# Kernel optimization log

Hardware: AMD Instinct MI355X
Metric: run time of the kernel (lower is better)

## Reference

```python
import jax, jax.numpy as jnp
import numpy as np

N, M, D = 8192, 8192, 512

def setup_inputs() -> dict:
    key = jax.random.key(0)
    kx, ky = jax.random.split(key)
    X = jax.random.normal(kx, (N, D), dtype=jnp.float32)
    Y = jax.random.normal(ky, (M, D), dtype=jnp.float32)
    gamma = jnp.float32(1.0)  # learnable scalar kernel width
    return {"X": X, "Y": Y, "gamma": gamma}

def reference(X, Y, gamma):
    # RBF kernel: exp(-gamma * ||x_i - y_j||^2)
    x2 = jnp.sum(X * X, axis=-1)            # [n]
    y2 = jnp.sum(Y * Y, axis=-1)            # [m]
    xy = jnp.einsum('nd,md->nm', X, Y)      # [n, m] GEMM
    sq = x2[:, None] + y2[None, :] - 2.0 * xy
    sq = jnp.maximum(sq, 0.0)               # clamp tiny negatives from fp error
    return jnp.exp(-gamma * sq)
```

## Files before the change

kernel.cpp:

```cpp
#include <hip/hip_runtime.h>
#include <hip/hip_bf16.h>


#define NROWS 8192
#define D_DIM 512
#define BM 256
#define BN 256
#define BK 64
#define NKT (D_DIM / BK)

using bf16x8 = __attribute__((ext_vector_type(8))) short;
using f32x4  = __attribute__((ext_vector_type(4))) float;

__device__ inline unsigned pack2_bf16(float a, float b) {
    unsigned ua = __builtin_bit_cast(unsigned, a);
    unsigned ub = __builtin_bit_cast(unsigned, b);
    ua = (ua + 0x7fffu + ((ua >> 16) & 1u)) >> 16;
    ub = (ub + 0x7fffu + ((ub >> 16) & 1u)) >> 16;
    return ua | (ub << 16);
}

__global__ __launch_bounds__(64) void prep_kernel(const float* __restrict__ src,
                                                  unsigned short* __restrict__ dst,
                                                  float* __restrict__ norms) {
    const int row  = blockIdx.x;
    const int lane = threadIdx.x;
    const float4* s = reinterpret_cast<const float4*>(src) + (size_t)row * (D_DIM / 4);
    float4 v0 = s[lane * 2];
    float4 v1 = s[lane * 2 + 1];
    float ss = v0.x * v0.x + v0.y * v0.y + v0.z * v0.z + v0.w * v0.w +
               v1.x * v1.x + v1.y * v1.y + v1.z * v1.z + v1.w * v1.w;
    uint4 p;
    p.x = pack2_bf16(v0.x, v0.y);
    p.y = pack2_bf16(v0.z, v0.w);
    p.z = pack2_bf16(v1.x, v1.y);
    p.w = pack2_bf16(v1.z, v1.w);
    reinterpret_cast<uint4*>(dst + (size_t)row * D_DIM)[lane] = p;
    #pragma unroll
    for (int off = 32; off; off >>= 1) ss += __shfl_down(ss, off);
    if (lane == 0) norms[row] = ss;
}

__device__ inline void gload_lds16(const unsigned short* g, unsigned short* l) {
    __builtin_amdgcn_global_load_lds(
        (const __attribute__((address_space(1))) void*)g,
        (__attribute__((address_space(3))) void*)l, 16, 0, 0);
}

#define VMCNT(n) asm volatile("s_waitcnt vmcnt(" #n ")" ::: "memory")
#define BAR()    asm volatile("s_barrier" ::: "memory")
#define LDF(p)   (*reinterpret_cast<const bf16x8*>(p))
#define MFMA(a, b, c) __builtin_amdgcn_mfma_f32_16x16x32_bf16(a, b, c, 0, 0, 0)

__global__ __launch_bounds__(512, 2) void rbf_gemm(
    const unsigned short* __restrict__ Xb, const unsigned short* __restrict__ Yb,
    const float* __restrict__ x2, const float* __restrict__ y2,
    const float* __restrict__ gptr, float* __restrict__ out) {
    __shared__ unsigned short sA[2][BM * BK];
    __shared__ unsigned short sB[2][BN * BK];

    const int bid  = blockIdx.x;
    const int swz  = (bid & 7) * 128 + (bid >> 3);
    const int brow = swz >> 5;
    const int bcol = swz & 31;

    const int tid  = threadIdx.x;
    const int lane = tid & 63;
    const int wid  = tid >> 6;
    const int wr   = wid >> 2;
    const int wc   = wid & 3;

    const int slot  = tid & 7;
    const int srowA = tid >> 3;
    const int srowB = ((tid >> 3) & 31) + ((tid >> 8) << 6);
    const int scol  = (slot ^ ((tid >> 3) & 7)) * 8;
    const unsigned short* gA = Xb + (size_t)(brow * BM + srowA) * D_DIM + scol;
    const unsigned short* gB = Yb + (size_t)(bcol * BN + srowB) * D_DIM + scol;
    const int loffA = srowA * BK + slot * 8;
    const int loffB = srowB * BK + slot * 8;

    auto stA = [&](int d, int kt, int odd) {
        const unsigned short* g = gA + (size_t)(odd * 64) * D_DIM + kt * BK;
        unsigned short* l = sA[d] + odd * 64 * BK + loffA;
        gload_lds16(g, l);
        gload_lds16(g + 128 * D_DIM, l + 128 * BK);
    };
    auto stB = [&](int d, int kt, int odd) {
        const unsigned short* g = gB + (size_t)(odd * 32) * D_DIM + kt * BK;
        unsigned short* l = sB[d] + odd * 32 * BK + loffB;
        gload_lds16(g, l);
        gload_lds16(g + 128 * D_DIM, l + 128 * BK);
    };

    const int lr  = lane & 15;
    const int kg  = lane >> 4;
    const int lx  = lane & 7;
    const int sl0 = ((0 * 4 + kg) ^ lx) * 8;
    const int sl1 = ((1 * 4 + kg) ^ lx) * 8;
    const int aBase = (wr * 128 + lr) * BK;
    const int bBase = (wc * 64 + lr) * BK;

    f32x4 acc[8][4] = {};
    bf16x8 av[4][2], bv[4][2];

    stA(0, 0, 0); stB(0, 0, 0); stB(0, 0, 1); stA(0, 0, 1);
    VMCNT(4);
    BAR();

    for (int t = 0; t < NKT; ++t) {
        const int c = t & 1, d = c ^ 1;
        const bool pre = (t + 1 < NKT);
        const unsigned short* A = sA[c];
        const unsigned short* B = sB[c];

        #pragma unroll
        for (int m = 0; m < 4; ++m) {
            av[m][0] = LDF(A + aBase + m * 16 * BK + sl0);
            av[m][1] = LDF(A + aBase + m * 16 * BK + sl1);
        }
        #pragma unroll
        for (int n = 0; n < 2; ++n) {
            bv[n][0] = LDF(B + bBase + n * 16 * BK + sl0);
            bv[n][1] = LDF(B + bBase + n * 16 * BK + sl1);
        }
        if (pre) { stA(d, t + 1, 0); VMCNT(4); }
        else     { VMCNT(2); }
        BAR();
        __builtin_amdgcn_s_setprio(1);
        #pragma unroll
        for (int m = 0; m < 4; ++m)
            #pragma unroll
            for (int n = 0; n < 2; ++n) {
                acc[m][n] = MFMA(av[m][0], bv[n][0], acc[m][n]);
                acc[m][n] = MFMA(av[m][1], bv[n][1], acc[m][n]);
            }
        __builtin_amdgcn_s_setprio(0);

        #pragma unroll
        for (int n = 2; n < 4; ++n) {
            bv[n][0] = LDF(B + bBase + n * 16 * BK + sl0);
            bv[n][1] = LDF(B + bBase + n * 16 * BK + sl1);
        }
        if (pre) { stB(d, t + 1, 0); VMCNT(4); }
        else     { VMCNT(0); }
        BAR();
        __builtin_amdgcn_s_setprio(1);
        #pragma unroll
        for (int m = 0; m < 4; ++m)
            #pragma unroll
            for (int n = 2; n < 4; ++n) {
                acc[m][n] = MFMA(av[m][0], bv[n][0], acc[m][n]);
                acc[m][n] = MFMA(av[m][1], bv[n][1], acc[m][n]);
            }
        __builtin_amdgcn_s_setprio(0);

        #pragma unroll
        for (int m = 0; m < 4; ++m) {
            av[m][0] = LDF(A + aBase + (m + 4) * 16 * BK + sl0);
            av[m][1] = LDF(A + aBase + (m + 4) * 16 * BK + sl1);
        }
        if (pre) stB(d, t + 1, 1);
        BAR();
        __builtin_amdgcn_s_setprio(1);
        #pragma unroll
        for (int m = 0; m < 4; ++m)
            #pragma unroll
            for (int n = 0; n < 2; ++n) {
                acc[m + 4][n] = MFMA(av[m][0], bv[n][0], acc[m + 4][n]);
                acc[m + 4][n] = MFMA(av[m][1], bv[n][1], acc[m + 4][n]);
            }
        __builtin_amdgcn_s_setprio(0);

        if (pre) {
            stA(d, t + 1, 1);
            VMCNT(4);
            BAR();
        }
        __builtin_amdgcn_s_setprio(1);
        #pragma unroll
        for (int m = 0; m < 4; ++m)
            #pragma unroll
            for (int n = 2; n < 4; ++n) {
                acc[m + 4][n] = MFMA(av[m][0], bv[n][0], acc[m + 4][n]);
                acc[m + 4][n] = MFMA(av[m][1], bv[n][1], acc[m + 4][n]);
            }
        __builtin_amdgcn_s_setprio(0);
    }

    const float g = *gptr;
    const int rbase = brow * BM + wr * 128 + (kg << 2);
    const int cbase = bcol * BN + wc * 64 + lr;

    float yv[4];
    #pragma unroll
    for (int n = 0; n < 4; ++n) yv[n] = y2[cbase + n * 16];

    #pragma unroll
    for (int m = 0; m < 8; ++m) {
        #pragma unroll
        for (int r = 0; r < 4; ++r) {
            const float xr = x2[rbase + m * 16 + r];
            const size_t ro = (size_t)(rbase + m * 16 + r) * NROWS + cbase;
            #pragma unroll
            for (int n = 0; n < 4; ++n) {
                float sq = fmaxf(xr + yv[n] - 2.0f * acc[m][n][r], 0.0f);
                __builtin_nontemporal_store(__expf(-g * sq), &out[ro + n * 16]);
            }
        }
    }
}

extern "C" void kernel_launch(void* const* d_in, const int* in_sizes, int n_in,
                              void* d_out, int out_size, void* d_ws, size_t ws_size,
                              hipStream_t stream) {
    const float* X = (const float*)d_in[0];
    const float* Y = (const float*)d_in[1];
    const float* gamma = (const float*)d_in[2];
    float* out = (float*)d_out;

    unsigned short* Xb = (unsigned short*)d_ws;
    unsigned short* Yb = Xb + (size_t)NROWS * D_DIM;
    float* x2 = (float*)(Yb + (size_t)NROWS * D_DIM);
    float* y2 = x2 + NROWS;

    prep_kernel<<<NROWS, 64, 0, stream>>>(X, Xb, x2);
    prep_kernel<<<NROWS, 64, 0, stream>>>(Y, Yb, y2);

    const int grid = (NROWS / BM) * (NROWS / BN);
    rbf_gemm<<<grid, 512, 0, stream>>>(Xb, Yb, x2, y2, gamma, out);
}
```

Baseline: 355.8 us.

## Deepen global-to-LDS prefetch pipeline and merge X/Y prep kernels

Reworks the GEMM main loop so LDS fills are issued as a flat stream of quarter-tile stages running seven stages ahead, instead of prefetching one k-tile inside the current iteration. Waits on outstanding loads now allow six in flight, which is meant to hide more global memory latency. Extra barriers are added after each MFMA quarter so a buffer is not overwritten while other waves still read it. Separately, the two prep launches are merged into one grid to save a launch. The added barriers and double buffering with a deeper prefetch distance risk both more sync overhead and read/write hazards.

```diff
diff --git a/kernel.cpp b/kernel.cpp
--- a/kernel.cpp
+++ b/kernel.cpp
@@ -20,10 +20,19 @@
     return ua | (ub << 16);
 }
 
-__global__ __launch_bounds__(64) void prep_kernel(const float* __restrict__ src,
-                                                  unsigned short* __restrict__ dst,
-                                                  float* __restrict__ norms) {
-    const int row  = blockIdx.x;
+__global__ __launch_bounds__(64) void prep_all(const float* __restrict__ X,
+                                               const float* __restrict__ Y,
+                                               unsigned short* __restrict__ Xb,
+                                               unsigned short* __restrict__ Yb,
+                                               float* __restrict__ x2,
+                                               float* __restrict__ y2) {
+    const int bid  = blockIdx.x;
+    const bool isY = bid >= NROWS;
+    const int row  = isY ? bid - NROWS : bid;
+    const float* src = isY ? Y : X;
+    unsigned short* dst = isY ? Yb : Xb;
+    float* nrm = isY ? y2 : x2;
+
     const int lane = threadIdx.x;
     const float4* s = reinterpret_cast<const float4*>(src) + (size_t)row * (D_DIM / 4);
     float4 v0 = s[lane * 2];
@@ -38,7 +47,7 @@
     reinterpret_cast<uint4*>(dst + (size_t)row * D_DIM)[lane] = p;
     #pragma unroll
     for (int off = 32; off; off >>= 1) ss += __shfl_down(ss, off);
-    if (lane == 0) norms[row] = ss;
+    if (lane == 0) nrm[row] = ss;
 }
 
 __device__ inline void gload_lds16(const unsigned short* g, unsigned short* l) {
@@ -91,6 +100,14 @@
         gload_lds16(g, l);
         gload_lds16(g + 128 * D_DIM, l + 128 * BK);
     };
+    auto STAGE_S = [&](int s) {
+        if (s >= 4 * NKT) return;
+        const int kt = s >> 2, ht = s & 3, d = kt & 1;
+        if      (ht == 0) stA(d, kt, 0);
+        else if (ht == 1) stB(d, kt, 0);
+        else if (ht == 2) stB(d, kt, 1);
+        else              stA(d, kt, 1);
+    };
 
     const int lr  = lane & 15;
     const int kg  = lane >> 4;
@@ -103,15 +120,16 @@
     f32x4 acc[8][4] = {};
     bf16x8 av[4][2], bv[4][2];
 
-    stA(0, 0, 0); stB(0, 0, 0); stB(0, 0, 1); stA(0, 0, 1);
-    VMCNT(4);
+    #pragma unroll
+    for (int s = 0; s < 7; ++s) STAGE_S(s);
+    VMCNT(6);
     BAR();
 
     for (int t = 0; t < NKT; ++t) {
-        const int c = t & 1, d = c ^ 1;
-        const bool pre = (t + 1 < NKT);
+        const int c = t & 1;
         const unsigned short* A = sA[c];
         const unsigned short* B = sB[c];
+        const int sbase = 7 + 4 * t;
 
         #pragma unroll
         for (int m = 0; m < 4; ++m) {
@@ -123,8 +141,7 @@
             bv[n][0] = LDF(B + bBase + n * 16 * BK + sl0);
             bv[n][1] = LDF(B + bBase + n * 16 * BK + sl1);
         }
-        if (pre) { stA(d, t + 1, 0); VMCNT(4); }
-        else     { VMCNT(2); }
+        STAGE_S(sbase);
         BAR();
         __builtin_amdgcn_s_setprio(1);
         #pragma unroll
@@ -135,14 +152,14 @@
                 acc[m][n] = MFMA(av[m][1], bv[n][1], acc[m][n]);
             }
         __builtin_amdgcn_s_setprio(0);
+        BAR();
 
         #pragma unroll
         for (int n = 2; n < 4; ++n) {
             bv[n][0] = LDF(B + bBase + n * 16 * BK + sl0);
             bv[n][1] = LDF(B + bBase + n * 16 * BK + sl1);
         }
-        if (pre) { stB(d, t + 1, 0); VMCNT(4); }
-        else     { VMCNT(0); }
+        STAGE_S(sbase + 1);
         BAR();
         __builtin_amdgcn_s_setprio(1);
         #pragma unroll
@@ -153,13 +170,14 @@
                 acc[m][n] = MFMA(av[m][1], bv[n][1], acc[m][n]);
             }
         __builtin_amdgcn_s_setprio(0);
+        BAR();
 
         #pragma unroll
         for (int m = 0; m < 4; ++m) {
             av[m][0] = LDF(A + aBase + (m + 4) * 16 * BK + sl0);
             av[m][1] = LDF(A + aBase + (m + 4) * 16 * BK + sl1);
         }
-        if (pre) stB(d, t + 1, 1);
+        STAGE_S(sbase + 2);
         BAR();
         __builtin_amdgcn_s_setprio(1);
         #pragma unroll
@@ -170,12 +188,12 @@
                 acc[m + 4][n] = MFMA(av[m][1], bv[n][1], acc[m + 4][n]);
             }
         __builtin_amdgcn_s_setprio(0);
-
-        if (pre) {
-            stA(d, t + 1, 1);
-            VMCNT(4);
-            BAR();
-        }
+        BAR();
+
+        STAGE_S(sbase + 3);
+        if (t < NKT - 2)       VMCNT(6);
+        else if (t == NKT - 2) VMCNT(0);
+        BAR();
         __builtin_amdgcn_s_setprio(1);
         #pragma unroll
         for (int m = 0; m < 4; ++m)
@@ -185,6 +203,7 @@
                 acc[m + 4][n] = MFMA(av[m][1], bv[n][1], acc[m + 4][n]);
             }
         __builtin_amdgcn_s_setprio(0);
+        BAR();
     }
 
     const float g = *gptr;
@@ -223,8 +242,7 @@
     float* x2 = (float*)(Yb + (size_t)NROWS * D_DIM);
     float* y2 = x2 + NROWS;
 
-    prep_kernel<<<NROWS, 64, 0, stream>>>(X, Xb, x2);
-    prep_kernel<<<NROWS, 64, 0, stream>>>(Y, Yb, y2);
+    prep_all<<<2 * NROWS, 64, 0, stream>>>(X, Y, Xb, Yb, x2, y2);
 
     const int grid = (NROWS / BM) * (NROWS / BN);
     rbf_gemm<<<grid, 512, 0, stream>>>(Xb, Yb, x2, y2, gamma, out);
```

After: 355.4 us. No clear change (-0.1%).
